# Kernel tuning notes

Hardware: AMD Instinct MI355X
Metric: run time of the kernel (lower is better)

Reference implementation:

```python
import jax, jax.numpy as jnp
import numpy as np

COMMITMENT_COST = 0.25


def setup_inputs() -> dict:
    key = jax.random.key(0)
    k1, k2 = jax.random.split(key)
    B, L, D, K = 32, 1024, 128, 1024
    z = jax.random.normal(k1, (B, L, D), dtype=jnp.float32)
    # torch init: uniform_(-1/num_embeddings, 1/num_embeddings)
    codebook = jax.random.uniform(k2, (K, D), dtype=jnp.float32,
                                  minval=-1.0 / K, maxval=1.0 / K)
    return {"z": z, "codebook": codebook}


def reference(z, codebook):
    D = codebook.shape[1]
    flat_z = z.reshape(-1, D)                         # [N, D]
    # squared-euclidean distances, expanded form (same math as torch)
    distances = (jnp.sum(flat_z ** 2, axis=1, keepdims=True)
                 + jnp.sum(codebook ** 2, axis=1)
                 - 2.0 * flat_z @ codebook.T)         # [N, K]
    encoding_indices = jnp.argmin(distances, axis=1)  # [N]
    quantized = codebook[encoding_indices].reshape(z.shape)
    # straight-through estimator
    z_q = z + jax.lax.stop_gradient(quantized - z)
    q_loss = jnp.mean((jax.lax.stop_gradient(quantized) - z) ** 2)
    e_loss = jnp.mean((quantized - jax.lax.stop_gradient(z)) ** 2)
    vq_loss = q_loss + COMMITMENT_COST * e_loss
    return z_q, vq_loss, encoding_indices
```

## Files before the change

### kernel.cpp

```cpp
#include <hip/hip_runtime.h>
#include <float.h>

#define NTOK 32768
#define DDIM 128
#define KCODES 1024
#define TT 128
#define NTHR 512
#define NCHUNK 16
#define CHUNK_BYTES 32768

typedef __attribute__((ext_vector_type(8))) short short8v;
typedef __attribute__((ext_vector_type(4))) float f32x4;

__device__ __forceinline__ float nofuse(float x) { asm volatile("" : "+v"(x)); return x; }

__device__ __forceinline__ unsigned short bf16rne(float x) {
    unsigned int u = __float_as_uint(x);
    unsigned int r = u + 0x7FFFu + ((u >> 16) & 1u);
    return (unsigned short)(r >> 16);
}
__device__ __forceinline__ float bf16tof(unsigned short h) {
    return __uint_as_float(((unsigned int)h) << 16);
}

__device__ __forceinline__ void cvt8(const float* f, uint4& hw, uint4& lw) {
    unsigned int h[8], l[8];
    #pragma unroll
    for (int e = 0; e < 8; ++e) {
        unsigned short hh = bf16rne(f[e]);
        unsigned short ll = bf16rne(f[e] - bf16tof(hh));
        h[e] = hh; l[e] = ll;
    }
    hw = make_uint4(h[0] | (h[1] << 16), h[2] | (h[3] << 16),
                    h[4] | (h[5] << 16), h[6] | (h[7] << 16));
    lw = make_uint4(l[0] | (l[1] << 16), l[2] | (l[3] << 16),
                    l[4] | (l[5] << 16), l[6] | (l[7] << 16));
}

__device__ __forceinline__ short8v as_s8(uint4 v) { return __builtin_bit_cast(short8v, v); }

__global__ __launch_bounds__(64)
void pack_cb(const float* __restrict__ cb, float* __restrict__ cnorm,
             char* __restrict__ cbS) {
    const int row = blockIdx.x * 64 + threadIdx.x;
    const float* p = cb + (size_t)row * DDIM;
    {
        float r[8];
        {
            float4 a = *(const float4*)p, c = *(const float4*)(p + 4);
            float v[8] = {a.x, a.y, a.z, a.w, c.x, c.y, c.z, c.w};
            #pragma unroll
            for (int j = 0; j < 8; ++j) r[j] = nofuse(v[j] * v[j]);
        }
        #pragma unroll
        for (int i = 8; i < DDIM; i += 8) {
            float4 a = *(const float4*)(p + i), c = *(const float4*)(p + i + 4);
            float v[8] = {a.x, a.y, a.z, a.w, c.x, c.y, c.z, c.w};
            #pragma unroll
            for (int j = 0; j < 8; ++j) r[j] = nofuse(r[j] + nofuse(v[j] * v[j]));
        }
        float s01 = nofuse(r[0] + r[1]), s23 = nofuse(r[2] + r[3]);
        float s45 = nofuse(r[4] + r[5]), s67 = nofuse(r[6] + r[7]);
        cnorm[row] = nofuse(nofuse(s01 + s23) + nofuse(s45 + s67));
    }
    char* base = cbS + (size_t)(row >> 6) * CHUNK_BYTES + (size_t)(row & 63) * 256;
    const int swz = (row & 7) << 4;
    #pragma unroll
    for (int d8 = 0; d8 < 16; ++d8) {
        float4 a = *(const float4*)(p + d8 * 8), c = *(const float4*)(p + d8 * 8 + 4);
        float f[8] = {a.x, a.y, a.z, a.w, c.x, c.y, c.z, c.w};
        uint4 hw, lw;
        cvt8(f, hw, lw);
        int col = (d8 << 4) ^ swz;
        *(uint4*)(base + col) = hw;
        *(uint4*)(base + 16384 + col) = lw;
    }
}

__global__ __launch_bounds__(NTHR, 2)
void dist_argmin(const float* __restrict__ z, const float* __restrict__ cb,
                 const float* __restrict__ cnorm, const char* __restrict__ cbS,
                 float* __restrict__ zq, float* __restrict__ idxf_out,
                 float* __restrict__ partials) {
    __shared__ __align__(16) char buf[2 * CHUNK_BYTES];
    __shared__ float zn_s[TT];
    __shared__ float cn_s[KCODES];
    __shared__ float red_v[TT * 4];
    __shared__ int   red_i[TT * 4];
    __shared__ int   bidx[TT];
    __shared__ float smf[8];

    const int tid  = threadIdx.x;
    const int lane = tid & 63;
    const int wave = tid >> 6;
    const int wy   = wave >> 2;
    const int wx   = wave & 3;
    const int l15  = lane & 15;
    const int l4   = lane >> 4;
    const int t0   = blockIdx.x * TT;

    auto stage = [&](int slot, int chunk) {
        const char* g = cbS + (size_t)chunk * CHUNK_BYTES + wave * 4096 + (lane << 4);
        char* ldst = buf + slot * CHUNK_BYTES + wave * 4096;
        #pragma unroll
        for (int j = 0; j < 4; ++j)
            __builtin_amdgcn_global_load_lds(
                (const __attribute__((address_space(1))) unsigned int*)(g + j * 1024),
                (__attribute__((address_space(3))) unsigned int*)(ldst + j * 1024),
                16, 0, 0);
    };

    short8v Ah[4][4], Al[4][4];
    #pragma unroll
    for (int tf = 0; tf < 4; ++tf) {
        int row = t0 + wy * 64 + tf * 16 + l15;
        const float* p = z + (size_t)row * DDIM;
        #pragma unroll
        for (int ks = 0; ks < 4; ++ks) {
            float4 a = *(const float4*)(p + ks * 32 + l4 * 8);
            float4 c = *(const float4*)(p + ks * 32 + l4 * 8 + 4);
            float f[8] = {a.x, a.y, a.z, a.w, c.x, c.y, c.z, c.w};
            uint4 hw, lw;
            cvt8(f, hw, lw);
            Ah[tf][ks] = as_s8(hw);
            Al[tf][ks] = as_s8(lw);
        }
    }

    stage(0, 0);

    cn_s[tid]       = cnorm[tid];
    cn_s[tid + 512] = cnorm[tid + 512];

    if (tid < TT) {
        const float* p = z + (size_t)(t0 + tid) * DDIM;
        float r[8];
        {
            float4 a = *(const float4*)p, c = *(const float4*)(p + 4);
            float v[8] = {a.x, a.y, a.z, a.w, c.x, c.y, c.z, c.w};
            #pragma unroll
            for (int j = 0; j < 8; ++j) r[j] = nofuse(v[j] * v[j]);
        }
        #pragma unroll
        for (int i = 8; i < DDIM; i += 8) {
            float4 a = *(const float4*)(p + i), c = *(const float4*)(p + i + 4);
            float v[8] = {a.x, a.y, a.z, a.w, c.x, c.y, c.z, c.w};
            #pragma unroll
            for (int j = 0; j < 8; ++j) r[j] = nofuse(r[j] + nofuse(v[j] * v[j]));
        }
        float s01 = nofuse(r[0] + r[1]), s23 = nofuse(r[2] + r[3]);
        float s45 = nofuse(r[4] + r[5]), s67 = nofuse(r[6] + r[7]);
        zn_s[tid] = nofuse(nofuse(s01 + s23) + nofuse(s45 + s67));
    }
    __syncthreads();

    float minv[16]; int mini[16];
    #pragma unroll
    for (int i = 0; i < 16; ++i) { minv[i] = FLT_MAX; mini[i] = 0; }

    auto compute = [&](int slot, int it) {
        const char* bb = buf + slot * CHUNK_BYTES;
        const int r = wx * 16 + l15;
        const int swz = (r & 7) << 4;
        const char* rowp = bb + r * 256;

        f32x4 acc[4];
        #pragma unroll
        for (int tf = 0; tf < 4; ++tf) acc[tf] = (f32x4){0.f, 0.f, 0.f, 0.f};

        #pragma unroll
        for (int ks = 0; ks < 4; ++ks) {
            int off = (((ks * 4 + l4) << 4)) ^ swz;
            short8v Bh = *(const short8v*)(rowp + off);
            short8v Bl = *(const short8v*)(rowp + 16384 + off);
            #pragma unroll
            for (int tf = 0; tf < 4; ++tf) {
                acc[tf] = __builtin_amdgcn_mfma_f32_16x16x32_bf16(Ah[tf][ks], Bh, acc[tf], 0, 0, 0);
                acc[tf] = __builtin_amdgcn_mfma_f32_16x16x32_bf16(Ah[tf][ks], Bl, acc[tf], 0, 0, 0);
                acc[tf] = __builtin_amdgcn_mfma_f32_16x16x32_bf16(Al[tf][ks], Bh, acc[tf], 0, 0, 0);
            }
        }

        int kk = it * 64 + wx * 16 + l15;
        float cn = cn_s[kk];
        #pragma unroll
        for (int tf = 0; tf < 4; ++tf)
            #pragma unroll
            for (int rg = 0; rg < 4; ++rg) {
                float zn = zn_s[wy * 64 + tf * 16 + l4 * 4 + rg];
                float s = nofuse(zn + cn);
                float dist = fmaf(-2.0f, acc[tf][rg], s);
                int ii = tf * 4 + rg;
                if (dist < minv[ii]) { minv[ii] = dist; mini[ii] = kk; }
            }
    };

    int cur = 0;
    #pragma unroll 1
    for (int t = 0; t < NCHUNK - 1; ++t) {
        stage(cur ^ 1, t + 1);
        asm volatile("s_waitcnt vmcnt(4)" ::: "memory");
        __builtin_amdgcn_s_barrier();
        compute(cur, t);
        asm volatile("s_waitcnt lgkmcnt(0)" ::: "memory");
        __builtin_amdgcn_s_barrier();
        cur ^= 1;
    }
    asm volatile("s_waitcnt vmcnt(0)" ::: "memory");
    __builtin_amdgcn_s_barrier();
    compute(cur, NCHUNK - 1);

    #pragma unroll
    for (int i = 0; i < 16; ++i) {
        float bv = minv[i]; int bi = mini[i];
        #pragma unroll
        for (int off = 1; off < 16; off <<= 1) {
            float ov = __shfl_xor(bv, off);
            int   oi = __shfl_xor(bi, off);
            if (ov < bv || (ov == bv && oi < bi)) { bv = ov; bi = oi; }
        }
        if (l15 == 0) {
            int tok = wy * 64 + (i >> 2) * 16 + l4 * 4 + (i & 3);
            red_v[tok * 4 + wx] = bv;
            red_i[tok * 4 + wx] = bi;
        }
    }
    __syncthreads();
    if (tid < TT) {
        float bv = red_v[tid * 4]; int bi = red_i[tid * 4];
        #pragma unroll
        for (int j = 1; j < 4; ++j) {
            float v = red_v[tid * 4 + j]; int ii = red_i[tid * 4 + j];
            if (v < bv || (v == bv && ii < bi)) { bv = v; bi = ii; }
        }
        bidx[tid] = bi;
        idxf_out[t0 + tid] = (float)bi;
    }
    __syncthreads();

    float s = 0.0f;
    #pragma unroll
    for (int ft = 0; ft < 8; ++ft) {
        int g = ft * NTHR + tid;
        int t = g >> 5;
        int d4 = g & 31;
        int k = bidx[t];
        float4 q4 = *(const float4*)(cb + (size_t)k * DDIM + 4 * d4);
        float4 z4 = *(const float4*)(z + (size_t)(t0 + t) * DDIM + 4 * d4);
        *(float4*)(zq + (size_t)(t0 + t) * DDIM + 4 * d4) = q4;
        float dx = q4.x - z4.x, dy = q4.y - z4.y, dz = q4.z - z4.z, dw = q4.w - z4.w;
        s += dx * dx + dy * dy + dz * dz + dw * dw;
    }
    #pragma unroll
    for (int off = 32; off > 0; off >>= 1) s += __shfl_down(s, off);
    if ((tid & 63) == 0) smf[tid >> 6] = s;
    __syncthreads();
    if (tid == 0) {
        float tot = 0.0f;
        #pragma unroll
        for (int w = 0; w < 8; ++w) tot += smf[w];
        partials[blockIdx.x] = tot;
    }
}

__global__ void loss_final(const float* __restrict__ partials, float* __restrict__ out_loss) {
    double s = 0.0;
    for (int i = threadIdx.x; i < NTOK / TT; i += 256) s += (double)partials[i];
    #pragma unroll
    for (int off = 32; off > 0; off >>= 1) s += __shfl_down(s, off);
    __shared__ double sm[4];
    int lane = threadIdx.x & 63, wv = threadIdx.x >> 6;
    if (lane == 0) sm[wv] = s;
    __syncthreads();
    if (threadIdx.x == 0) {
        double tot = sm[0] + sm[1] + sm[2] + sm[3];
        out_loss[0] = (float)(tot * 1.25 / (double)((size_t)NTOK * DDIM));
    }
}

extern "C" void kernel_launch(void* const* d_in, const int* in_sizes, int n_in,
                              void* d_out, int out_size, void* d_ws, size_t ws_size,
                              hipStream_t stream) {
    const float* z  = (const float*)d_in[0];
    const float* cb = (const float*)d_in[1];
    float* out = (float*)d_out;
    float* zq   = out;
    float* loss = out + (size_t)NTOK * DDIM;
    float* idxf = loss + 1;

    float* cnorm    = (float*)d_ws;
    float* partials = cnorm + KCODES;
    char*  cbS      = (char*)(partials + 256);

    pack_cb<<<KCODES / 64, 64, 0, stream>>>(cb, cnorm, cbS);
    dist_argmin<<<NTOK / TT, NTHR, 0, stream>>>(z, cb, cnorm, cbS, zq, idxf, partials);
    loss_final<<<1, 256, 0, stream>>>(partials, loss);
}
```

Measured before the change: 122.4 us.

## Halve token tile, raise occupancy, and fuse loss reduction into last block

```diff
diff --git a/kernel.cpp b/kernel.cpp
--- a/kernel.cpp
+++ b/kernel.cpp
@@ -4,10 +4,11 @@
 #define NTOK 32768
 #define DDIM 128
 #define KCODES 1024
-#define TT 128
+#define TT 64
 #define NTHR 512
 #define NCHUNK 16
 #define CHUNK_BYTES 32768
+#define NBLK (NTOK / TT)
 
 typedef __attribute__((ext_vector_type(8))) short short8v;
 typedef __attribute__((ext_vector_type(4))) float f32x4;
@@ -41,7 +42,8 @@
 
 __global__ __launch_bounds__(64)
 void pack_cb(const float* __restrict__ cb, float* __restrict__ cnorm,
-             char* __restrict__ cbS) {
+             char* __restrict__ cbS, int* __restrict__ done_ctr) {
+    if (blockIdx.x == 0 && threadIdx.x == 0) *done_ctr = 0;
     const int row = blockIdx.x * 64 + threadIdx.x;
     const float* p = cb + (size_t)row * DDIM;
     {
@@ -77,11 +79,12 @@
     }
 }
 
-__global__ __launch_bounds__(NTHR, 2)
+__global__ __launch_bounds__(NTHR, 4)
 void dist_argmin(const float* __restrict__ z, const float* __restrict__ cb,
                  const float* __restrict__ cnorm, const char* __restrict__ cbS,
                  float* __restrict__ zq, float* __restrict__ idxf_out,
-                 float* __restrict__ partials) {
+                 float* __restrict__ partials, int* __restrict__ done_ctr,
+                 float* __restrict__ out_loss) {
     __shared__ __align__(16) char buf[2 * CHUNK_BYTES];
     __shared__ float zn_s[TT];
     __shared__ float cn_s[KCODES];
@@ -89,6 +92,7 @@
     __shared__ int   red_i[TT * 4];
     __shared__ int   bidx[TT];
     __shared__ float smf[8];
+    __shared__ int   lastflag;
 
     const int tid  = threadIdx.x;
     const int lane = tid & 63;
@@ -110,10 +114,10 @@
                 16, 0, 0);
     };
 
-    short8v Ah[4][4], Al[4][4];
-    #pragma unroll
-    for (int tf = 0; tf < 4; ++tf) {
-        int row = t0 + wy * 64 + tf * 16 + l15;
+    short8v Ah[2][4], Al[2][4];
+    #pragma unroll
+    for (int tf = 0; tf < 2; ++tf) {
+        int row = t0 + wy * 32 + tf * 16 + l15;
         const float* p = z + (size_t)row * DDIM;
         #pragma unroll
         for (int ks = 0; ks < 4; ++ks) {
@@ -154,9 +158,16 @@
     }
     __syncthreads();
 
-    float minv[16]; int mini[16];
-    #pragma unroll
-    for (int i = 0; i < 16; ++i) { minv[i] = FLT_MAX; mini[i] = 0; }
+    float znr[8];
+    #pragma unroll
+    for (int tf = 0; tf < 2; ++tf)
+        #pragma unroll
+        for (int rg = 0; rg < 4; ++rg)
+            znr[tf * 4 + rg] = zn_s[wy * 32 + tf * 16 + l4 * 4 + rg];
+
+    float minv[8]; int mini[8];
+    #pragma unroll
+    for (int i = 0; i < 8; ++i) { minv[i] = FLT_MAX; mini[i] = 0; }
 
     auto compute = [&](int slot, int it) {
         const char* bb = buf + slot * CHUNK_BYTES;
@@ -164,9 +175,9 @@
         const int swz = (r & 7) << 4;
         const char* rowp = bb + r * 256;
 
-        f32x4 acc[4];
-        #pragma unroll
-        for (int tf = 0; tf < 4; ++tf) acc[tf] = (f32x4){0.f, 0.f, 0.f, 0.f};
+        f32x4 acc[2];
+        #pragma unroll
+        for (int tf = 0; tf < 2; ++tf) acc[tf] = (f32x4){0.f, 0.f, 0.f, 0.f};
 
         #pragma unroll
         for (int ks = 0; ks < 4; ++ks) {
@@ -174,7 +185,7 @@
             short8v Bh = *(const short8v*)(rowp + off);
             short8v Bl = *(const short8v*)(rowp + 16384 + off);
             #pragma unroll
-            for (int tf = 0; tf < 4; ++tf) {
+            for (int tf = 0; tf < 2; ++tf) {
                 acc[tf] = __builtin_amdgcn_mfma_f32_16x16x32_bf16(Ah[tf][ks], Bh, acc[tf], 0, 0, 0);
                 acc[tf] = __builtin_amdgcn_mfma_f32_16x16x32_bf16(Ah[tf][ks], Bl, acc[tf], 0, 0, 0);
                 acc[tf] = __builtin_amdgcn_mfma_f32_16x16x32_bf16(Al[tf][ks], Bh, acc[tf], 0, 0, 0);
@@ -184,11 +195,10 @@
         int kk = it * 64 + wx * 16 + l15;
         float cn = cn_s[kk];
         #pragma unroll
-        for (int tf = 0; tf < 4; ++tf)
+        for (int tf = 0; tf < 2; ++tf)
             #pragma unroll
             for (int rg = 0; rg < 4; ++rg) {
-                float zn = zn_s[wy * 64 + tf * 16 + l4 * 4 + rg];
-                float s = nofuse(zn + cn);
+                float s = nofuse(znr[tf * 4 + rg] + cn);
                 float dist = fmaf(-2.0f, acc[tf][rg], s);
                 int ii = tf * 4 + rg;
                 if (dist < minv[ii]) { minv[ii] = dist; mini[ii] = kk; }
@@ -211,7 +221,7 @@
     compute(cur, NCHUNK - 1);
 
     #pragma unroll
-    for (int i = 0; i < 16; ++i) {
+    for (int i = 0; i < 8; ++i) {
         float bv = minv[i]; int bi = mini[i];
         #pragma unroll
         for (int off = 1; off < 16; off <<= 1) {
@@ -220,7 +230,7 @@
             if (ov < bv || (ov == bv && oi < bi)) { bv = ov; bi = oi; }
         }
         if (l15 == 0) {
-            int tok = wy * 64 + (i >> 2) * 16 + l4 * 4 + (i & 3);
+            int tok = wy * 32 + (i >> 2) * 16 + l4 * 4 + (i & 3);
             red_v[tok * 4 + wx] = bv;
             red_i[tok * 4 + wx] = bi;
         }
@@ -240,7 +250,7 @@
 
     float s = 0.0f;
     #pragma unroll
-    for (int ft = 0; ft < 8; ++ft) {
+    for (int ft = 0; ft < 4; ++ft) {
         int g = ft * NTHR + tid;
         int t = g >> 5;
         int d4 = g & 31;
@@ -255,26 +265,26 @@
     for (int off = 32; off > 0; off >>= 1) s += __shfl_down(s, off);
     if ((tid & 63) == 0) smf[tid >> 6] = s;
     __syncthreads();
-    if (tid == 0) {
-        float tot = 0.0f;
-        #pragma unroll
-        for (int w = 0; w < 8; ++w) tot += smf[w];
-        partials[blockIdx.x] = tot;
-    }
-}
-
-__global__ void loss_final(const float* __restrict__ partials, float* __restrict__ out_loss) {
-    double s = 0.0;
-    for (int i = threadIdx.x; i < NTOK / TT; i += 256) s += (double)partials[i];
-    #pragma unroll
-    for (int off = 32; off > 0; off >>= 1) s += __shfl_down(s, off);
-    __shared__ double sm[4];
-    int lane = threadIdx.x & 63, wv = threadIdx.x >> 6;
-    if (lane == 0) sm[wv] = s;
-    __syncthreads();
-    if (threadIdx.x == 0) {
-        double tot = sm[0] + sm[1] + sm[2] + sm[3];
-        out_loss[0] = (float)(tot * 1.25 / (double)((size_t)NTOK * DDIM));
+    if (tid == 0) partials[blockIdx.x] = smf[0] + smf[1] + smf[2] + smf[3]
+                                       + smf[4] + smf[5] + smf[6] + smf[7];
+
+    __threadfence();
+    if (tid == 0) lastflag = (atomicAdd(done_ctr, 1) == NBLK - 1);
+    __syncthreads();
+    if (lastflag) {
+        __threadfence();
+        double d = (double)partials[tid];
+        #pragma unroll
+        for (int off = 32; off > 0; off >>= 1) d += __shfl_down(d, off);
+        __shared__ double smd[8];
+        if ((tid & 63) == 0) smd[tid >> 6] = d;
+        __syncthreads();
+        if (tid == 0) {
+            double tot = 0.0;
+            #pragma unroll
+            for (int w = 0; w < 8; ++w) tot += smd[w];
+            out_loss[0] = (float)(tot * 1.25 / (double)((size_t)NTOK * DDIM));
+        }
     }
 }
 
@@ -290,9 +300,10 @@
 
     float* cnorm    = (float*)d_ws;
     float* partials = cnorm + KCODES;
-    char*  cbS      = (char*)(partials + 256);
-
-    pack_cb<<<KCODES / 64, 64, 0, stream>>>(cb, cnorm, cbS);
-    dist_argmin<<<NTOK / TT, NTHR, 0, stream>>>(z, cb, cnorm, cbS, zq, idxf, partials);
-    loss_final<<<1, 256, 0, stream>>>(partials, loss);
-}
+    int*   done_ctr = (int*)(partials + NBLK);
+    char*  cbS      = (char*)(done_ctr + 4);
+
+    pack_cb<<<KCODES / 64, 64, 0, stream>>>(cb, cnorm, cbS, done_ctr);
+    dist_argmin<<<NBLK, NTHR, 0, stream>>>(z, cb, cnorm, cbS, zq, idxf,
+                                           partials, done_ctr, loss);
+}
```

Measured after the change: 209.4 us. +71.0%, slower.
